# Kernel optimization log

Measured on AMD Instinct MI355X. Metric: run time of the kernel, lower is better.

The kernel has to match this reference:

```python
import jax, jax.numpy as jnp
import numpy as np

M, K, N = 8192, 4096, 4096
ALPHA, BETA = 0.002, 0.0005


def setup_inputs() -> dict:
    key = jax.random.key(0)
    kx, kw, kb = jax.random.split(key, 3)
    # int8-range quantized activations and weights (stored as int32 for portability)
    x = jax.random.randint(kx, (M, K), -127, 127, dtype=jnp.int32)
    weight = jax.random.randint(kw, (N, K), -127, 127, dtype=jnp.int32)  # (out, in)
    bias = jax.random.randint(kb, (1, N), -(2**20), 2**20, dtype=jnp.int32)
    alpha = jnp.float32(ALPHA)
    beta = jnp.float32(BETA)
    return {"x": x, "weight": weight, "bias": bias, "alpha": alpha, "beta": beta}


def reference(x, weight, bias, alpha, beta):
    # int8 GEMM with int32 accumulation: acc[m, n] = sum_k x[m, k] * W[n, k]
    acc = jnp.matmul(x, weight.T, preferred_element_type=jnp.int32)  # [M, N] int32
    # CUTLASS-style epilogue: D = round(alpha * acc + beta * bias) -> int32
    y = alpha * acc.astype(jnp.float32) + beta * bias.astype(jnp.float32)
    return jnp.round(y).astype(jnp.int32)
```

## Files before the change

### kernel.cpp

```cpp
#include <hip/hip_runtime.h>
#include <hip/hip_bf16.h>
#include <stdint.h>

#define M_DIM 8192
#define N_DIM 4096
#define K_DIM 4096

#define BM 256
#define BN 256
#define BK 64
#define NT (K_DIM / BK)
#define DEPTH 4

typedef int v4i __attribute__((ext_vector_type(4)));

#define AS1C(p) ((const __attribute__((address_space(1))) void*)(p))
#define AS3(p)  ((__attribute__((address_space(3))) void*)(p))

__device__ __forceinline__ int pack4(int a, int b, int c, int d) {
  return (a & 0xff) | ((b & 0xff) << 8) | ((c & 0xff) << 16) | (d << 24);
}

__global__ void pack_both_kernel(const int* __restrict__ x, const int* __restrict__ w,
                                 char* __restrict__ A8, char* __restrict__ B8,
                                 int nA, int nTot) {
  int idx = blockIdx.x * blockDim.x + threadIdx.x;
  int stride = gridDim.x * blockDim.x;
  for (int i = idx; i < nTot; i += stride) {
    const int4* pin;
    int4* pout;
    if (i < nA) {
      pin  = (const int4*)x + 4 * (size_t)i;
      pout = (int4*)A8 + i;
    } else {
      int j = i - nA;
      pin  = (const int4*)w + 4 * (size_t)j;
      pout = (int4*)B8 + j;
    }
    int4 v0 = pin[0];
    int4 v1 = pin[1];
    int4 v2 = pin[2];
    int4 v3 = pin[3];
    int4 o;
    o.x = pack4(v0.x, v0.y, v0.z, v0.w);
    o.y = pack4(v1.x, v1.y, v1.z, v1.w);
    o.z = pack4(v2.x, v2.y, v2.z, v2.w);
    o.w = pack4(v3.x, v3.y, v3.z, v3.w);
    *pout = o;
  }
}

__global__ __launch_bounds__(512, 2) void gemm_i8_kernel(
    const char* __restrict__ A8, const char* __restrict__ B8,
    const int* __restrict__ bias, const float* __restrict__ alpha_p,
    const float* __restrict__ beta_p, int* __restrict__ out) {
  __shared__ alignas(16) char lds[DEPTH][BM * BK + BN * BK];

  const int tid  = threadIdx.x;
  const int lane = tid & 63;
  const int wave = tid >> 6;

  const int orig = blockIdx.x;
  const int swz  = (orig & 7) * (512 / 8) + (orig >> 3);
  const int bm   = (swz >> 4) * BM;
  const int bn   = (swz & 15) * BN;

  int aoff[2], boff[2], ldsoff[2];
#pragma unroll
  for (int i = 0; i < 2; ++i) {
    int linear = i * 8192 + tid * 16;
    int row = linear >> 6;
    int p   = (linear >> 4) & 3;
    int g   = p ^ ((row >> 1) & 3);
    ldsoff[i] = i * 8192 + wave * 1024;
    aoff[i] = (bm + row) * K_DIM + g * 16;
    boff[i] = (bn + row) * K_DIM + g * 16;
  }

#define STAGE_A(t)                                                                  \
  do {                                                                              \
    const char* ab_ = A8 + (t) * BK;                                                \
    char* base_ = &lds[(t) & (DEPTH - 1)][0];                                       \
    _Pragma("unroll") for (int i_ = 0; i_ < 2; ++i_)                                \
      __builtin_amdgcn_global_load_lds(AS1C(ab_ + aoff[i_]),                        \
                                       AS3(base_ + ldsoff[i_]), 16, 0, 0);          \
  } while (0)

#define STAGE_B(t)                                                                  \
  do {                                                                              \
    const char* bb_ = B8 + (t) * BK;                                                \
    char* base_ = &lds[(t) & (DEPTH - 1)][0];                                       \
    _Pragma("unroll") for (int i_ = 0; i_ < 2; ++i_)                                \
      __builtin_amdgcn_global_load_lds(AS1C(bb_ + boff[i_]),                        \
                                       AS3(base_ + 16384 + ldsoff[i_]), 16, 0, 0);  \
  } while (0)

  v4i acc[8][4];
#pragma unroll
  for (int i = 0; i < 8; ++i)
#pragma unroll
    for (int j = 0; j < 4; ++j) acc[i][j] = (v4i){0, 0, 0, 0};

  const int wr = wave >> 2;
  const int wc = wave & 3;
  const int frow = lane & 15;
  const int fchunk = lane >> 4;
  const int swzoff = ((fchunk ^ ((frow >> 1) & 3)) << 4);

  v4i bf[4], aflo[4], afhi[4];

#define READ0(t)                                                                    \
  do {                                                                              \
    const char* base_ = &lds[(t) & (DEPTH - 1)][0];                                 \
    _Pragma("unroll") for (int nj = 0; nj < 4; ++nj)                                \
      bf[nj] = *(const v4i*)(base_ + 16384 + (wc * 64 + nj * 16 + frow) * 64 +      \
                             swzoff);                                               \
    _Pragma("unroll") for (int mi = 0; mi < 4; ++mi)                                \
      aflo[mi] = *(const v4i*)(base_ + (wr * 128 + mi * 16 + frow) * 64 + swzoff);  \
  } while (0)

#define READ1(t)                                                                    \
  do {                                                                              \
    const char* base_ = &lds[(t) & (DEPTH - 1)][0];                                 \
    _Pragma("unroll") for (int mi = 0; mi < 4; ++mi)                                \
      afhi[mi] = *(const v4i*)(base_ + (wr * 128 + (mi + 4) * 16 + frow) * 64 +     \
                               swzoff);                                             \
  } while (0)

#define MFMA_LO()                                                                   \
  do {                                                                              \
    __builtin_amdgcn_s_setprio(1);                                                  \
    _Pragma("unroll") for (int mi = 0; mi < 4; ++mi)                                \
      _Pragma("unroll") for (int nj = 0; nj < 4; ++nj)                              \
        acc[mi][nj] = __builtin_amdgcn_mfma_i32_16x16x64_i8(aflo[mi], bf[nj],       \
                                                            acc[mi][nj], 0, 0, 0); \
    __builtin_amdgcn_s_setprio(0);                                                  \
  } while (0)

#define MFMA_HI()                                                                   \
  do {                                                                              \
    __builtin_amdgcn_s_setprio(1);                                                  \
    _Pragma("unroll") for (int mi = 0; mi < 4; ++mi)                                \
      _Pragma("unroll") for (int nj = 0; nj < 4; ++nj)                              \
        acc[mi + 4][nj] = __builtin_amdgcn_mfma_i32_16x16x64_i8(afhi[mi], bf[nj],   \
                                                                acc[mi + 4][nj],   \
                                                                0, 0, 0);          \
    __builtin_amdgcn_s_setprio(0);                                                  \
  } while (0)

#define PHASE0(t, DO_STAGE)                                                         \
  do {                                                                              \
    READ0(t);                                                                       \
    if (DO_STAGE) STAGE_A((t) + 3);                                                 \
    __builtin_amdgcn_s_barrier();                                                   \
    asm volatile("s_waitcnt lgkmcnt(0)" ::: "memory");                              \
    MFMA_LO();                                                                      \
    __builtin_amdgcn_s_barrier();                                                   \
  } while (0)

#define PHASE1(t, DO_STAGE)                                                         \
  do {                                                                              \
    READ1(t);                                                                       \
    if (DO_STAGE) STAGE_B((t) + 3);                                                 \
    __builtin_amdgcn_s_barrier();                                                   \
    asm volatile("s_waitcnt lgkmcnt(0)" ::: "memory");                              \
    MFMA_HI();                                                                      \
  } while (0)

  STAGE_A(0); STAGE_B(0);
  STAGE_A(1); STAGE_B(1);
  STAGE_A(2); STAGE_B(2);
  asm volatile("s_waitcnt vmcnt(8)" ::: "memory");
  __builtin_amdgcn_s_barrier();

  for (int t = 0; t < NT - 3; ++t) {
    PHASE0(t, true);
    PHASE1(t, true);
    asm volatile("s_waitcnt vmcnt(8)" ::: "memory");
    __builtin_amdgcn_s_barrier();
  }
  PHASE0(NT - 3, false);
  PHASE1(NT - 3, false);
  asm volatile("s_waitcnt vmcnt(4)" ::: "memory");
  __builtin_amdgcn_s_barrier();
  PHASE0(NT - 2, false);
  PHASE1(NT - 2, false);
  asm volatile("s_waitcnt vmcnt(0)" ::: "memory");
  __builtin_amdgcn_s_barrier();
  PHASE0(NT - 1, false);
  PHASE1(NT - 1, false);

  const float alpha = *alpha_p;
  const float beta  = *beta_p;
  const int col0 = bn + wc * 64 + frow;
  float bb4[4];
#pragma unroll
  for (int nj = 0; nj < 4; ++nj) bb4[nj] = beta * (float)bias[col0 + nj * 16];

  const int rbase = bm + wr * 128 + (lane >> 4) * 4;
#pragma unroll
  for (int mi = 0; mi < 8; ++mi) {
#pragma unroll
    for (int r = 0; r < 4; ++r) {
      size_t rowoff = (size_t)(rbase + mi * 16 + r) * N_DIM;
#pragma unroll
      for (int nj = 0; nj < 4; ++nj) {
        out[rowoff + col0 + nj * 16] =
            (int)rintf(fmaf(alpha, (float)acc[mi][nj][r], bb4[nj]));
      }
    }
  }
#undef STAGE_A
#undef STAGE_B
#undef READ0
#undef READ1
#undef MFMA_LO
#undef MFMA_HI
#undef PHASE0
#undef PHASE1
}

__global__ void naive_kernel(const int* __restrict__ x, const int* __restrict__ w,
                             const int* __restrict__ bias,
                             const float* __restrict__ alpha_p,
                             const float* __restrict__ beta_p,
                             int* __restrict__ out) {
  size_t idx = (size_t)blockIdx.x * 256 + threadIdx.x;
  int m = (int)(idx / N_DIM);
  int n = (int)(idx % N_DIM);
  const int4* xr = (const int4*)(x + (size_t)m * K_DIM);
  const int4* wr = (const int4*)(w + (size_t)n * K_DIM);
  int acc = 0;
  for (int k = 0; k < K_DIM / 4; ++k) {
    int4 a = xr[k];
    int4 b = wr[k];
    acc += a.x * b.x + a.y * b.y + a.z * b.z + a.w * b.w;
  }
  out[idx] = (int)rintf(fmaf(*alpha_p, (float)acc, (*beta_p) * (float)bias[n]));
}

extern "C" void kernel_launch(void* const* d_in, const int* in_sizes, int n_in,
                              void* d_out, int out_size, void* d_ws, size_t ws_size,
                              hipStream_t stream) {
  const int*   x     = (const int*)d_in[0];
  const int*   w     = (const int*)d_in[1];
  const int*   bias  = (const int*)d_in[2];
  const float* alpha = (const float*)d_in[3];
  const float* beta  = (const float*)d_in[4];
  int* out = (int*)d_out;

  const size_t a8_bytes = (size_t)M_DIM * K_DIM;
  const size_t b8_bytes = (size_t)N_DIM * K_DIM;

  if (ws_size >= a8_bytes + b8_bytes) {
    char* A8 = (char*)d_ws;
    char* B8 = A8 + a8_bytes;
    const int nA = (int)(a8_bytes / 16);
    const int nTot = (int)((a8_bytes + b8_bytes) / 16);
    pack_both_kernel<<<2048, 256, 0, stream>>>(x, w, A8, B8, nA, nTot);
    const int nblk = (M_DIM / BM) * (N_DIM / BN);
    gemm_i8_kernel<<<nblk, 512, 0, stream>>>(A8, B8, bias, alpha, beta, out);
  } else {
    naive_kernel<<<(M_DIM * (size_t)N_DIM) / 256, 256, 0, stream>>>(x, w, bias, alpha, beta, out);
  }
}
```

Before: 187.9 us.

## Software-pipeline LDS fragment reads across tiles and drop mid-tile barriers

Replaces the two-phase-per-tile schedule, which had a barrier and an lgkmcnt(0) wait before each MFMA half, with one TILE step per k-tile. Each step issues the next tile's B and A-low fragment reads while the current tile's MFMA_HI runs, and alternates between two register sets. Global-to-LDS staging is interleaved between the MFMA halves, and the step ends with a single vmcnt wait and barrier. The aim is to hide LDS read latency behind matrix ops and cut barrier stalls, at the cost of more live VGPRs and a fragile tail and wait-count schedule.

```diff
diff --git a/kernel.cpp b/kernel.cpp
--- a/kernel.cpp
+++ b/kernel.cpp
@@ -107,16 +107,17 @@
   const int fchunk = lane >> 4;
   const int swzoff = ((fchunk ^ ((frow >> 1) & 3)) << 4);
 
-  v4i bf[4], aflo[4], afhi[4];
-
-#define READ0(t)                                                                    \
+  v4i bf0[4], aflo0[4], bf1[4], aflo1[4], afhi[4];
+
+#define READ0(S, t)                                                                 \
   do {                                                                              \
     const char* base_ = &lds[(t) & (DEPTH - 1)][0];                                 \
     _Pragma("unroll") for (int nj = 0; nj < 4; ++nj)                                \
-      bf[nj] = *(const v4i*)(base_ + 16384 + (wc * 64 + nj * 16 + frow) * 64 +      \
-                             swzoff);                                               \
-    _Pragma("unroll") for (int mi = 0; mi < 4; ++mi)                                \
-      aflo[mi] = *(const v4i*)(base_ + (wr * 128 + mi * 16 + frow) * 64 + swzoff);  \
+      bf##S[nj] = *(const v4i*)(base_ + 16384 + (wc * 64 + nj * 16 + frow) * 64 +   \
+                                swzoff);                                            \
+    _Pragma("unroll") for (int mi = 0; mi < 4; ++mi)                                \
+      aflo##S[mi] = *(const v4i*)(base_ + (wr * 128 + mi * 16 + frow) * 64 +        \
+                                  swzoff);                                          \
   } while (0)
 
 #define READ1(t)                                                                    \
@@ -127,68 +128,55 @@
                                swzoff);                                             \
   } while (0)
 
-#define MFMA_LO()                                                                   \
+#define MFMA_LO(S)                                                                  \
   do {                                                                              \
     __builtin_amdgcn_s_setprio(1);                                                  \
     _Pragma("unroll") for (int mi = 0; mi < 4; ++mi)                                \
       _Pragma("unroll") for (int nj = 0; nj < 4; ++nj)                              \
-        acc[mi][nj] = __builtin_amdgcn_mfma_i32_16x16x64_i8(aflo[mi], bf[nj],       \
+        acc[mi][nj] = __builtin_amdgcn_mfma_i32_16x16x64_i8(aflo##S[mi], bf##S[nj], \
                                                             acc[mi][nj], 0, 0, 0); \
     __builtin_amdgcn_s_setprio(0);                                                  \
   } while (0)
 
-#define MFMA_HI()                                                                   \
+#define MFMA_HI(S)                                                                  \
   do {                                                                              \
     __builtin_amdgcn_s_setprio(1);                                                  \
     _Pragma("unroll") for (int mi = 0; mi < 4; ++mi)                                \
       _Pragma("unroll") for (int nj = 0; nj < 4; ++nj)                              \
-        acc[mi + 4][nj] = __builtin_amdgcn_mfma_i32_16x16x64_i8(afhi[mi], bf[nj],   \
+        acc[mi + 4][nj] = __builtin_amdgcn_mfma_i32_16x16x64_i8(afhi[mi], bf##S[nj],\
                                                                 acc[mi + 4][nj],   \
                                                                 0, 0, 0);          \
     __builtin_amdgcn_s_setprio(0);                                                  \
   } while (0)
 
-#define PHASE0(t, DO_STAGE)                                                         \
-  do {                                                                              \
-    READ0(t);                                                                       \
-    if (DO_STAGE) STAGE_A((t) + 3);                                                 \
-    __builtin_amdgcn_s_barrier();                                                   \
-    asm volatile("s_waitcnt lgkmcnt(0)" ::: "memory");                              \
-    MFMA_LO();                                                                      \
-    __builtin_amdgcn_s_barrier();                                                   \
-  } while (0)
-
-#define PHASE1(t, DO_STAGE)                                                         \
-  do {                                                                              \
+#define TILE(t, C, N, STG, EV)                                                      \
+  do {                                                                              \
+    if (STG) STAGE_A((t) + 3);                                                      \
     READ1(t);                                                                       \
-    if (DO_STAGE) STAGE_B((t) + 3);                                                 \
-    __builtin_amdgcn_s_barrier();                                                   \
-    asm volatile("s_waitcnt lgkmcnt(0)" ::: "memory");                              \
-    MFMA_HI();                                                                      \
+    MFMA_LO(C);                                                                     \
+    if (STG) STAGE_B((t) + 3);                                                      \
+    if ((t) + 1 < NT) READ0(N, (t) + 1);                                            \
+    MFMA_HI(C);                                                                     \
+    if ((EV) == 4) asm volatile("s_waitcnt vmcnt(4)" ::: "memory");                 \
+    if ((EV) == 0) asm volatile("s_waitcnt vmcnt(0)" ::: "memory");                 \
+    if ((EV) >= 0) __builtin_amdgcn_s_barrier();                                    \
   } while (0)
 
   STAGE_A(0); STAGE_B(0);
   STAGE_A(1); STAGE_B(1);
   STAGE_A(2); STAGE_B(2);
-  asm volatile("s_waitcnt vmcnt(8)" ::: "memory");
-  __builtin_amdgcn_s_barrier();
-
-  for (int t = 0; t < NT - 3; ++t) {
-    PHASE0(t, true);
-    PHASE1(t, true);
-    asm volatile("s_waitcnt vmcnt(8)" ::: "memory");
-    __builtin_amdgcn_s_barrier();
-  }
-  PHASE0(NT - 3, false);
-  PHASE1(NT - 3, false);
   asm volatile("s_waitcnt vmcnt(4)" ::: "memory");
   __builtin_amdgcn_s_barrier();
-  PHASE0(NT - 2, false);
-  PHASE1(NT - 2, false);
-  asm volatile("s_waitcnt vmcnt(0)" ::: "memory");
-  __builtin_amdgcn_s_barrier();
-  PHASE0(NT - 1, false);
-  PHASE1(NT - 1, false);
+  READ0(0, 0);
+
+  for (int t = 0; t < NT - 4; t += 2) {
+    TILE(t, 0, 1, true, 4);
+    TILE(t + 1, 1, 0, true, 4);
+  }
+  TILE(NT - 4, 0, 1, true, 4);
+  TILE(NT - 3, 1, 0, false, 0);
+  TILE(NT - 2, 0, 1, false, -1);
+  TILE(NT - 1, 1, 0, false, -1);
 
   const float alpha = *alpha_p;
   const float beta  = *beta_p;
@@ -216,8 +204,7 @@
 #undef READ1
 #undef MFMA_LO
 #undef MFMA_HI
-#undef PHASE0
-#undef PHASE1
+#undef TILE
 }
 
 __global__ void naive_kernel(const int* __restrict__ x, const int* __restrict__ w,
```

Measured after the change: 182.1 us. 1.03x faster.
